# Kernel optimization log

Measured on AMD Instinct MI355X. Metric: run time of the kernel, lower is better.

Reference implementation:

```python
import jax, jax.numpy as jnp
import numpy as np

BS, D, NC, N, C, K = 8192, 1024, 64, 100000, 1000, 50


def setup_inputs() -> dict:
    key = jax.random.key(0)
    k1, k2, k3, k4, k5 = jax.random.split(key, 5)
    return {
        "train_embedding": jax.random.normal(k1, (BS, D), dtype=jnp.float32),
        # concept initialized uniform in [-0.5, 0.5] as in init_concept
        "concept": jax.random.uniform(k2, (D, NC), dtype=jnp.float32, minval=-0.5, maxval=0.5),
        "bank": jax.random.normal(k3, (N, D), dtype=jnp.float32),
        "W_h": jax.random.normal(k4, (D, C), dtype=jnp.float32) * 0.02,
        "b_h": jax.random.normal(k5, (C,), dtype=jnp.float32) * 0.02,
        "topk": K,
    }


def reference(train_embedding, concept, bank, W_h, b_h, topk):
    # h_x: linear classifier head
    def h_x(z):
        return z @ W_h + b_h

    # projection onto concept subspace: C (C^T C)^{-1} C^T
    G = concept.T @ concept                      # [nc, nc]
    proj_matrix = concept @ jnp.linalg.inv(G) @ concept.T  # [D, D]
    proj = train_embedding @ proj_matrix.T       # (proj_matrix @ X^T)^T -> [bs, D]
    y_pred = h_x(proj)                           # [bs, C]
    orig_pred = h_x(train_embedding)             # [bs, C]

    # batched per-concept Euclidean distance to the whole bank: [nc, N]
    bank_sq = jnp.sum(bank * bank, axis=1)       # [N]
    con_sq = jnp.sum(concept * concept, axis=0)  # [nc]
    d2 = con_sq[:, None] - 2.0 * (concept.T @ bank.T) + bank_sq[None, :]
    dist = jnp.sqrt(jnp.maximum(d2, 0.0))
    # topk SMALLEST distances per concept
    _, idx = jax.lax.top_k(-dist, topk)          # idx: [nc, k]
    knn = bank[idx]                              # [nc, k, D] gather

    # L_sparse_1: mean over concepts of (c . mean_k knn)
    dots = jnp.einsum('dn,nkd->n', concept, knn) / topk  # [nc]
    L_sparse_1 = jnp.mean(dots)

    nc = concept.shape[1]
    eye = jnp.eye(nc, dtype=concept.dtype)
    L_sparse_2 = jnp.mean(G * (1.0 - eye))       # off-diagonal mean
    norm_metrics = jnp.mean(G * eye)             # diagonal mean

    return (orig_pred, y_pred, L_sparse_1, L_sparse_2, norm_metrics)
```

## Files before the change

### kernel.cpp

```cpp
#include <hip/hip_runtime.h>
#include <cstddef>

#define BSZ   8192
#define DIM   1024
#define NCON  64
#define NBANK 100000
#define NCLS  1000
#define TOPK  50
#define NCHUNK 32
#define CHUNK  3125
#define CHUNKP 3328

#define Y_OFF 8192000
#define S_OFF 16384000

typedef __attribute__((ext_vector_type(8))) short bf16x8;
typedef __attribute__((ext_vector_type(4))) float f32x4;

__device__ __forceinline__ short f2bf(float x) {
    unsigned u = __builtin_bit_cast(unsigned, x);
    unsigned r = (u + 0x7fffu + ((u >> 16) & 1u)) >> 16;
    return (short)r;
}

__device__ __forceinline__ bf16x8 pack8(f32x4 a, f32x4 b) {
    bf16x8 p;
    p[0] = f2bf(a[0]); p[1] = f2bf(a[1]); p[2] = f2bf(a[2]); p[3] = f2bf(a[3]);
    p[4] = f2bf(b[0]); p[5] = f2bf(b[1]); p[6] = f2bf(b[2]); p[7] = f2bf(b[3]);
    return p;
}

__device__ __forceinline__ void gload16(const short* g, short* l) {
    __builtin_amdgcn_global_load_lds(
        (__attribute__((address_space(1))) void*)g,
        (__attribute__((address_space(3))) void*)l,
        16, 0, 0);
}

__global__ void __launch_bounds__(256) prep_kernel(const float* __restrict__ cpt,
                                                   const float* __restrict__ Wh,
                                                   short* __restrict__ WcatT,
                                                   short* __restrict__ cptT,
                                                   short* __restrict__ cptR) {
    __shared__ short Ts[64][65];
    int b = blockIdx.x;
    int t = threadIdx.x;
    if (b < 256) {
        int k0 = (b & 15) * 64, n0 = (b >> 4) * 64;
        #pragma unroll
        for (int i = 0; i < 16; ++i) {
            int u = i * 256 + t;
            int kL = u >> 6, nL = u & 63;
            int n = n0 + nL;
            Ts[kL][nL] = (n < NCLS) ? f2bf(Wh[(size_t)(k0 + kL) * NCLS + n]) : (short)0;
        }
        __syncthreads();
        #pragma unroll
        for (int i = 0; i < 16; ++i) {
            int u = i * 256 + t;
            int nL = u >> 6, kL = u & 63;
            WcatT[(size_t)(n0 + nL) * DIM + k0 + kL] = Ts[kL][nL];
        }
    } else {
        int q = b - 256;
        #pragma unroll
        for (int i = 0; i < 16; ++i) {
            int u = q * 4096 + i * 256 + t;
            int d = u >> 6, n = u & 63;
            short v = f2bf(cpt[u]);
            cptR[u] = v;
            cptT[n * DIM + d] = v;
        }
    }
}

__global__ void __launch_bounds__(256) mid_kernel(const float* __restrict__ bank,
                                                  const float* __restrict__ X,
                                                  const short* __restrict__ cptT,
                                                  const short* __restrict__ WcatT,
                                                  short* __restrict__ Xbf,
                                                  float* __restrict__ key,
                                                  float* __restrict__ bank_sq,
                                                  float* __restrict__ M,
                                                  float* __restrict__ G,
                                                  float* __restrict__ invG) {
    __shared__ float rowk[64];
    __shared__ float fk[64];
    int b = blockIdx.x;
    int t = threadIdx.x;
    int wid = t >> 6, l = t & 63, lr = l & 15, lg = l >> 4;
    if (b < 782) {
        int j0 = b * 128;
        int j_[2]; bool v_[2];
        const float* brow[2];
        #pragma unroll
        for (int ni = 0; ni < 2; ++ni) {
            j_[ni] = j0 + wid * 32 + ni * 16 + lr;
            v_[ni] = j_[ni] < NBANK;
            brow[ni] = bank + (size_t)j_[ni] * DIM + lg * 8;
        }
        f32x4 acc[4][2] = {};
        float sq[2] = {0.f, 0.f};
        for (int kk = 0; kk < DIM; kk += 32) {
            bf16x8 af[4];
            #pragma unroll
            for (int mi = 0; mi < 4; ++mi)
                af[mi] = *(const bf16x8*)(cptT + (mi * 16 + lr) * DIM + kk + lg * 8);
            #pragma unroll
            for (int ni = 0; ni < 2; ++ni) {
                f32x4 a = v_[ni] ? *(const f32x4*)(brow[ni] + kk)     : f32x4{0.f, 0.f, 0.f, 0.f};
                f32x4 c = v_[ni] ? *(const f32x4*)(brow[ni] + kk + 4) : f32x4{0.f, 0.f, 0.f, 0.f};
                sq[ni] += a[0]*a[0] + a[1]*a[1] + a[2]*a[2] + a[3]*a[3]
                        + c[0]*c[0] + c[1]*c[1] + c[2]*c[2] + c[3]*c[3];
                bf16x8 bfr = pack8(a, c);
                #pragma unroll
                for (int mi = 0; mi < 4; ++mi)
                    acc[mi][ni] = __builtin_amdgcn_mfma_f32_16x16x32_bf16(af[mi], bfr, acc[mi][ni], 0, 0, 0);
            }
        }
        #pragma unroll
        for (int ni = 0; ni < 2; ++ni) {
            float s = sq[ni];
            s += __shfl_xor(s, 16);
            s += __shfl_xor(s, 32);
            sq[ni] = s;
            if (v_[ni] && lg == 0) bank_sq[j_[ni]] = s;
        }
        #pragma unroll
        for (int mi = 0; mi < 4; ++mi)
            #pragma unroll
            for (int ni = 0; ni < 2; ++ni)
                if (v_[ni]) {
                    #pragma unroll
                    for (int r = 0; r < 4; ++r) {
                        int m = mi * 16 + lg * 4 + r;
                        key[(size_t)m * NBANK + j_[ni]] = sq[ni] - 2.f * acc[mi][ni][r];
                    }
                }
    } else if (b < 790) {
        int c0 = (b - 782) * 128;
        f32x4 acc[4][2] = {};
        for (int kk = 0; kk < DIM; kk += 32) {
            bf16x8 af[4], bfr[2];
            #pragma unroll
            for (int mi = 0; mi < 4; ++mi)
                af[mi] = *(const bf16x8*)(cptT + (mi * 16 + lr) * DIM + kk + lg * 8);
            #pragma unroll
            for (int ni = 0; ni < 2; ++ni)
                bfr[ni] = *(const bf16x8*)(WcatT + (size_t)(c0 + wid * 32 + ni * 16 + lr) * DIM + kk + lg * 8);
            #pragma unroll
            for (int mi = 0; mi < 4; ++mi)
                #pragma unroll
                for (int ni = 0; ni < 2; ++ni)
                    acc[mi][ni] = __builtin_amdgcn_mfma_f32_16x16x32_bf16(af[mi], bfr[ni], acc[mi][ni], 0, 0, 0);
        }
        #pragma unroll
        for (int mi = 0; mi < 4; ++mi)
            #pragma unroll
            for (int ni = 0; ni < 2; ++ni)
                #pragma unroll
                for (int r = 0; r < 4; ++r)
                    M[(mi * 16 + lg * 4 + r) * 1024 + c0 + wid * 32 + ni * 16 + lr] = acc[mi][ni][r];
    } else if (b == 790) {
        f32x4 acc[4] = {};
        for (int kk = 0; kk < DIM; kk += 32) {
            bf16x8 af[4], bfr;
            #pragma unroll
            for (int mi = 0; mi < 4; ++mi)
                af[mi] = *(const bf16x8*)(cptT + (mi * 16 + lr) * DIM + kk + lg * 8);
            bfr = *(const bf16x8*)(cptT + (wid * 16 + lr) * DIM + kk + lg * 8);
            #pragma unroll
            for (int mi = 0; mi < 4; ++mi)
                acc[mi] = __builtin_amdgcn_mfma_f32_16x16x32_bf16(af[mi], bfr, acc[mi], 0, 0, 0);
        }
        #pragma unroll
        for (int mi = 0; mi < 4; ++mi)
            #pragma unroll
            for (int r = 0; r < 4; ++r)
                G[(mi * 16 + lg * 4 + r) * 64 + wid * 16 + lr] = acc[mi][r];
        __syncthreads();
        float myA[16];
        #pragma unroll
        for (int s = 0; s < 16; ++s) myA[s] = G[(4 * s + wid) * 64 + l];
        #pragma unroll
        for (int k = 0; k < 64; ++k) {
            if (wid == (k & 3)) rowk[l] = myA[k >> 2];
            if (l == k) {
                #pragma unroll
                for (int s = 0; s < 16; ++s) fk[4 * s + wid] = myA[s];
            }
            __syncthreads();
            float ip = 1.f / rowk[k];
            float rv = rowk[l];
            #pragma unroll
            for (int s = 0; s < 16; ++s) {
                int i = 4 * s + wid;
                float fv = fk[i];
                float nv;
                if (i == k && l == k)      nv = ip;
                else if (i == k)           nv = rv * ip;
                else if (l == k)           nv = -fv * ip;
                else                       nv = myA[s] - fv * (rv * ip);
                myA[s] = nv;
            }
            __syncthreads();
        }
        #pragma unroll
        for (int s = 0; s < 16; ++s) invG[(4 * s + wid) * 64 + l] = myA[s];
    } else {
        size_t u = ((size_t)(b - 791) * 256 + t) * 8;
        f32x4 a = *(const f32x4*)(X + u);
        f32x4 c = *(const f32x4*)(X + u + 4);
        *(bf16x8*)(Xbf + u) = pack8(a, c);
    }
}

__global__ void __launch_bounds__(256) topA_kernel(const float* __restrict__ key,
                                                   float* __restrict__ cand_v,
                                                   int* __restrict__ cand_j) {
    int n = blockIdx.x >> 5;
    int c = blockIdx.x & 31;
    int base = c * CHUNK;
    const float* row = key + (size_t)n * NBANK + base;
    __shared__ float vals[CHUNKP];
    __shared__ float wv[4];
    __shared__ int wj[4];
    int t = threadIdx.x;
    float lv = __builtin_inff();
    int lj = 0x7fffffff;
    #pragma unroll 13
    for (int i = 0; i < 13; ++i) {
        int j = t + i * 256;
        float v = (j < CHUNK) ? row[j] : __builtin_inff();
        vals[j] = v;
        if (v < lv) { lv = v; lj = j; }
    }
    __syncthreads();
    float* cv = cand_v + (size_t)blockIdx.x * TOPK;
    int* cj = cand_j + (size_t)blockIdx.x * TOPK;
    for (int it = 0; it < TOPK; ++it) {
        float bv = lv; int bj = lj;
        #pragma unroll
        for (int o = 32; o > 0; o >>= 1) {
            float ov = __shfl_down(bv, o);
            int oj = __shfl_down(bj, o);
            if (ov < bv || (ov == bv && oj < bj)) { bv = ov; bj = oj; }
        }
        if ((t & 63) == 0) { wv[t >> 6] = bv; wj[t >> 6] = bj; }
        __syncthreads();
        float gv = wv[0]; int gj = wj[0];
        #pragma unroll
        for (int w = 1; w < 4; ++w)
            if (wv[w] < gv || (wv[w] == gv && wj[w] < gj)) { gv = wv[w]; gj = wj[w]; }
        if (t == 0) { cv[it] = gv; cj[it] = base + gj; }
        if (t == (gj & 255)) {
            vals[gj] = __builtin_inff();
            lv = __builtin_inff(); lj = 0x7fffffff;
            #pragma unroll 13
            for (int i = 0; i < 13; ++i) {
                int j = t + i * 256;
                float v = vals[j];
                if (v < lv) { lv = v; lj = j; }
            }
        }
        __syncthreads();
    }
}

__global__ void __launch_bounds__(256) m2w2_topB_kernel(const float* __restrict__ invG,
                                                        const float* __restrict__ M,
                                                        const short* __restrict__ cptR,
                                                        short* __restrict__ WcatT,
                                                        const float* __restrict__ cand_v,
                                                        const int* __restrict__ cand_j,
                                                        const float* __restrict__ bank_sq,
                                                        float* __restrict__ dots) {
    __shared__ __align__(16) char smem[49408];
    int b = blockIdx.x;
    int t = threadIdx.x;
    if (b < 8) {
        float* Mt = (float*)smem;
        short* M2s = (short*)(smem + 33024);
        int c0 = b * 128;
        for (int u = t; u < 8192; u += 256) {
            int j = u >> 7, cc = u & 127;
            Mt[j * 129 + cc] = M[j * 1024 + c0 + cc];
        }
        __syncthreads();
        int cl = t & 127, half = t >> 7;
        for (int nn = 0; nn < 32; ++nn) {
            int n = half * 32 + nn;
            float a = 0.f;
            #pragma unroll 16
            for (int j = 0; j < 64; ++j) a += invG[n * 64 + j] * Mt[j * 129 + cl];
            int s = n >> 3;
            M2s[cl * 64 + (((s ^ (cl & 7)) << 3) | (n & 7))] = f2bf(a);
        }
        __syncthreads();
        int wid = t >> 6, l = t & 63, lr = l & 15, lg = l >> 4;
        int wr = wid >> 1, wc = wid & 1;
        for (int d0 = 0; d0 < DIM; d0 += 128) {
            f32x4 acc[4][4] = {};
            #pragma unroll
            for (int ks = 0; ks < 2; ++ks) {
                bf16x8 af[4], bfr[4];
                #pragma unroll
                for (int mi = 0; mi < 4; ++mi) {
                    int rr = wr * 64 + mi * 16 + lr;
                    int slot = (ks * 4 + lg) ^ (rr & 7);
                    af[mi] = *(const bf16x8*)(M2s + rr * 64 + slot * 8);
                }
                #pragma unroll
                for (int ni = 0; ni < 4; ++ni)
                    bfr[ni] = *(const bf16x8*)(cptR + (size_t)(d0 + wc * 64 + ni * 16 + lr) * 64 + ks * 32 + lg * 8);
                #pragma unroll
                for (int mi = 0; mi < 4; ++mi)
                    #pragma unroll
                    for (int ni = 0; ni < 4; ++ni)
                        acc[mi][ni] = __builtin_amdgcn_mfma_f32_16x16x32_bf16(af[mi], bfr[ni], acc[mi][ni], 0, 0, 0);
            }
            #pragma unroll
            for (int mi = 0; mi < 4; ++mi)
                #pragma unroll
                for (int ni = 0; ni < 4; ++ni)
                    #pragma unroll
                    for (int r = 0; r < 4; ++r) {
                        int cc = c0 + wr * 64 + mi * 16 + lg * 4 + r;
                        int d = d0 + wc * 64 + ni * 16 + lr;
                        WcatT[(size_t)(1024 + cc) * DIM + d] = f2bf(acc[mi][ni][r]);
                    }
        }
    } else {
        int n = b - 8;
        const int NC2 = NCHUNK * TOPK;
        float* vals = (float*)smem;
        int* gidx = (int*)(smem + 6400);
        float* wv = (float*)(smem + 12800);
        int* wj = (int*)(smem + 12816);
        int* wl = (int*)(smem + 12832);
        for (int j = t; j < NC2; j += 256) {
            vals[j] = cand_v[(size_t)n * NC2 + j];
            gidx[j] = cand_j[(size_t)n * NC2 + j];
        }
        __syncthreads();
        float sum = 0.f;
        for (int it = 0; it < TOPK; ++it) {
            float bv = __builtin_inff();
            int bj = 0x7fffffff;
            int bl = -1;
            #pragma unroll 7
            for (int j = t; j < NC2; j += 256) {
                float v = vals[j];
                int gj = gidx[j];
                if (v < bv || (v == bv && gj < bj)) { bv = v; bj = gj; bl = j; }
            }
            #pragma unroll
            for (int o = 32; o > 0; o >>= 1) {
                float ov = __shfl_down(bv, o);
                int oj = __shfl_down(bj, o);
                int ol = __shfl_down(bl, o);
                if (ov < bv || (ov == bv && oj < bj)) { bv = ov; bj = oj; bl = ol; }
            }
            if ((t & 63) == 0) { wv[t >> 6] = bv; wj[t >> 6] = bj; wl[t >> 6] = bl; }
            __syncthreads();
            if (t == 0) {
                #pragma unroll
                for (int w = 1; w < 4; ++w)
                    if (wv[w] < bv || (wv[w] == bv && wj[w] < bj)) { bv = wv[w]; bj = wj[w]; bl = wl[w]; }
                sum += 0.5f * (bank_sq[bj] - bv);
                vals[bl] = __builtin_inff();
            }
            __syncthreads();
        }
        if (t == 0) dots[n] = sum / (float)TOPK;
    }
}

__global__ void __launch_bounds__(256) pred_fin_kernel(const short* __restrict__ Xbf,
                                                       const short* __restrict__ WcatT,
                                                       const float* __restrict__ bh,
                                                       const float* __restrict__ G,
                                                       const float* __restrict__ dots,
                                                       float* __restrict__ orig,
                                                       float* __restrict__ ypred,
                                                       float* __restrict__ out3) {
    __shared__ __align__(16) char smem[32768];
    int b = blockIdx.x;
    int t = threadIdx.x;
    if (b < 1024) {
        short* As = (short*)smem;
        short* Bs = (short*)(smem + 16384);
        int c0 = (b & 15) * 128;
        int r0 = (b >> 4) * 128;
        int wid = t >> 6, l = t & 63, lr = l & 15, lg = l >> 4;
        int wr = wid >> 1, wc = wid & 1;
        int srow_off = l >> 3;
        int scol = ((l & 7) ^ (l >> 3)) * 8;
        f32x4 acc[4][4] = {};
        for (int kk = 0; kk < DIM; kk += 64) {
            if (kk) __syncthreads();
            #pragma unroll
            for (int i = 0; i < 4; ++i) {
                int si = wid * 4 + i;
                int row = si * 8 + srow_off;
                gload16(Xbf + (size_t)(r0 + row) * DIM + kk + scol, As + si * 512);
                gload16(WcatT + (size_t)(c0 + row) * DIM + kk + scol, Bs + si * 512);
            }
            __syncthreads();
            #pragma unroll
            for (int ks = 0; ks < 2; ++ks) {
                bf16x8 af[4], bfr[4];
                #pragma unroll
                for (int mi = 0; mi < 4; ++mi) {
                    int rr = wr * 64 + mi * 16 + lr;
                    int slot = (ks * 4 + lg) ^ (rr & 7);
                    af[mi] = *(const bf16x8*)(As + rr * 64 + slot * 8);
                }
                #pragma unroll
                for (int ni = 0; ni < 4; ++ni) {
                    int cc = wc * 64 + ni * 16 + lr;
                    int slot = (ks * 4 + lg) ^ (cc & 7);
                    bfr[ni] = *(const bf16x8*)(Bs + cc * 64 + slot * 8);
                }
                #pragma unroll
                for (int mi = 0; mi < 4; ++mi)
                    #pragma unroll
                    for (int ni = 0; ni < 4; ++ni)
                        acc[mi][ni] = __builtin_amdgcn_mfma_f32_16x16x32_bf16(af[mi], bfr[ni], acc[mi][ni], 0, 0, 0);
            }
        }
        #pragma unroll
        for (int mi = 0; mi < 4; ++mi)
            #pragma unroll
            for (int ni = 0; ni < 4; ++ni) {
                int cg = c0 + wc * 64 + ni * 16 + lr;
                bool isorig = cg < NCLS;
                bool isy = (cg >= 1024) && (cg < 1024 + NCLS);
                if (isorig || isy) {
                    int cl = isorig ? cg : cg - 1024;
                    float bias = bh[cl];
                    float* dst = isorig ? orig : ypred;
                    #pragma unroll
                    for (int r = 0; r < 4; ++r) {
                        int row = r0 + wr * 64 + mi * 16 + lg * 4 + r;
                        dst[(size_t)row * NCLS + cl] = acc[mi][ni][r] + bias;
                    }
                }
            }
    } else {
        float* r1 = (float*)smem;
        float* r2 = (float*)(smem + 1024);
        float* r3 = (float*)(smem + 2048);
        float sd = 0.f, so = 0.f;
        for (int u = t; u < 4096; u += 256) {
            float g = G[u];
            if ((u >> 6) == (u & 63)) sd += g; else so += g;
        }
        float s1 = (t < NCON) ? dots[t] : 0.f;
        r1[t] = sd; r2[t] = so; r3[t] = s1;
        __syncthreads();
        for (int o = 128; o > 0; o >>= 1) {
            if (t < o) { r1[t] += r1[t + o]; r2[t] += r2[t + o]; r3[t] += r3[t + o]; }
            __syncthreads();
        }
        if (t == 0) {
            out3[0] = r3[0] / 64.f;
            out3[1] = r2[0] / 4096.f;
            out3[2] = r1[0] / 4096.f;
        }
    }
}

extern "C" void kernel_launch(void* const* d_in, const int* in_sizes, int n_in,
                              void* d_out, int out_size, void* d_ws, size_t ws_size,
                              hipStream_t stream) {
    const float* X    = (const float*)d_in[0];
    const float* cpt  = (const float*)d_in[1];
    const float* bank = (const float*)d_in[2];
    const float* Wh   = (const float*)d_in[3];
    const float* bh   = (const float*)d_in[4];
    float* out = (float*)d_out;

    float* orig  = out;
    float* ypred = out + Y_OFF;
    float* out3  = out + S_OFF;

    char* w = (char*)d_ws;
    short* Xbf    = (short*)(w);
    short* WcatT  = (short*)(w + 16777216);
    short* cptT   = (short*)(w + 20971520);
    short* cptR   = (short*)(w + 21102592);
    float* key    = (float*)(w + 21233664);
    float* bank_sq= (float*)(w + 46833664);
    float* G      = (float*)(w + 47234048);
    float* invG   = (float*)(w + 47250432);
    float* M      = (float*)(w + 47266816);
    float* cand_v = (float*)(w + 47528960);
    int*   cand_j = (int*)  (w + 47938560);
    float* dots   = (float*)(w + 48348160);

    prep_kernel<<<272, 256, 0, stream>>>(cpt, Wh, WcatT, cptT, cptR);
    mid_kernel<<<4887, 256, 0, stream>>>(bank, X, cptT, WcatT, Xbf, key, bank_sq, M, G, invG);
    topA_kernel<<<NCON * NCHUNK, 256, 0, stream>>>(key, cand_v, cand_j);
    m2w2_topB_kernel<<<72, 256, 0, stream>>>(invG, M, cptR, WcatT, cand_v, cand_j, bank_sq, dots);
    pred_fin_kernel<<<1025, 256, 0, stream>>>(Xbf, WcatT, bh, G, dots, orig, ypred, out3);
}
```

Baseline: 424.8 us.

## Compute y_pred via low-rank X·C then (invG·M) instead of a full D-wide projected GEMM

Instead of building a 1024-wide projected weight block (C·invG·C^T·W_h) and running the prediction GEMM over 2048 output columns, the code now computes X·C (rank 64) inside the X-to-bf16 conversion blocks. y_pred then comes from a small K=64 GEMM against invG·M. This roughly halves the big GEMM work, and the M2 computation is folded into the topA launch. It adds another bf16 rounding of the intermediate X·C and one extra small kernel launch for the final reductions.

```diff
diff --git a/kernel.cpp b/kernel.cpp
--- a/kernel.cpp
+++ b/kernel.cpp
@@ -39,9 +39,8 @@
 
 __global__ void __launch_bounds__(256) prep_kernel(const float* __restrict__ cpt,
                                                    const float* __restrict__ Wh,
-                                                   short* __restrict__ WcatT,
-                                                   short* __restrict__ cptT,
-                                                   short* __restrict__ cptR) {
+                                                   short* __restrict__ WhT,
+                                                   short* __restrict__ cptT) {
     __shared__ short Ts[64][65];
     int b = blockIdx.x;
     int t = threadIdx.x;
@@ -59,7 +58,7 @@
         for (int i = 0; i < 16; ++i) {
             int u = i * 256 + t;
             int nL = u >> 6, kL = u & 63;
-            WcatT[(size_t)(n0 + nL) * DIM + k0 + kL] = Ts[kL][nL];
+            WhT[(size_t)(n0 + nL) * DIM + k0 + kL] = Ts[kL][nL];
         }
     } else {
         int q = b - 256;
@@ -67,9 +66,7 @@
         for (int i = 0; i < 16; ++i) {
             int u = q * 4096 + i * 256 + t;
             int d = u >> 6, n = u & 63;
-            short v = f2bf(cpt[u]);
-            cptR[u] = v;
-            cptT[n * DIM + d] = v;
+            cptT[n * DIM + d] = f2bf(cpt[u]);
         }
     }
 }
@@ -77,8 +74,9 @@
 __global__ void __launch_bounds__(256) mid_kernel(const float* __restrict__ bank,
                                                   const float* __restrict__ X,
                                                   const short* __restrict__ cptT,
-                                                  const short* __restrict__ WcatT,
+                                                  const short* __restrict__ WhT,
                                                   short* __restrict__ Xbf,
+                                                  short* __restrict__ XCbf,
                                                   float* __restrict__ key,
                                                   float* __restrict__ bank_sq,
                                                   float* __restrict__ M,
@@ -147,7 +145,7 @@
                 af[mi] = *(const bf16x8*)(cptT + (mi * 16 + lr) * DIM + kk + lg * 8);
             #pragma unroll
             for (int ni = 0; ni < 2; ++ni)
-                bfr[ni] = *(const bf16x8*)(WcatT + (size_t)(c0 + wid * 32 + ni * 16 + lr) * DIM + kk + lg * 8);
+                bfr[ni] = *(const bf16x8*)(WhT + (size_t)(c0 + wid * 32 + ni * 16 + lr) * DIM + kk + lg * 8);
             #pragma unroll
             for (int mi = 0; mi < 4; ++mi)
                 #pragma unroll
@@ -208,80 +206,102 @@
         #pragma unroll
         for (int s = 0; s < 16; ++s) invG[(4 * s + wid) * 64 + l] = myA[s];
     } else {
-        size_t u = ((size_t)(b - 791) * 256 + t) * 8;
-        f32x4 a = *(const f32x4*)(X + u);
-        f32x4 c = *(const f32x4*)(X + u + 4);
-        *(bf16x8*)(Xbf + u) = pack8(a, c);
+        int r0 = (b - 791) * 128;
+        int r_[2];
+        const float* xrow[2];
+        #pragma unroll
+        for (int ni = 0; ni < 2; ++ni) {
+            r_[ni] = r0 + wid * 32 + ni * 16 + lr;
+            xrow[ni] = X + (size_t)r_[ni] * DIM + lg * 8;
+        }
+        f32x4 acc[4][2] = {};
+        for (int kk = 0; kk < DIM; kk += 32) {
+            bf16x8 af[4];
+            #pragma unroll
+            for (int mi = 0; mi < 4; ++mi)
+                af[mi] = *(const bf16x8*)(cptT + (mi * 16 + lr) * DIM + kk + lg * 8);
+            #pragma unroll
+            for (int ni = 0; ni < 2; ++ni) {
+                f32x4 a = *(const f32x4*)(xrow[ni] + kk);
+                f32x4 c = *(const f32x4*)(xrow[ni] + kk + 4);
+                bf16x8 pk = pack8(a, c);
+                *(bf16x8*)(Xbf + (size_t)r_[ni] * DIM + kk + lg * 8) = pk;
+                #pragma unroll
+                for (int mi = 0; mi < 4; ++mi)
+                    acc[mi][ni] = __builtin_amdgcn_mfma_f32_16x16x32_bf16(af[mi], pk, acc[mi][ni], 0, 0, 0);
+            }
+        }
+        #pragma unroll
+        for (int mi = 0; mi < 4; ++mi)
+            #pragma unroll
+            for (int ni = 0; ni < 2; ++ni)
+                #pragma unroll
+                for (int r = 0; r < 4; ++r) {
+                    int m = mi * 16 + lg * 4 + r;
+                    XCbf[(size_t)r_[ni] * NCON + m] = f2bf(acc[mi][ni][r]);
+                }
     }
 }
 
 __global__ void __launch_bounds__(256) topA_kernel(const float* __restrict__ key,
                                                    float* __restrict__ cand_v,
-                                                   int* __restrict__ cand_j) {
-    int n = blockIdx.x >> 5;
-    int c = blockIdx.x & 31;
-    int base = c * CHUNK;
-    const float* row = key + (size_t)n * NBANK + base;
-    __shared__ float vals[CHUNKP];
-    __shared__ float wv[4];
-    __shared__ int wj[4];
-    int t = threadIdx.x;
-    float lv = __builtin_inff();
-    int lj = 0x7fffffff;
-    #pragma unroll 13
-    for (int i = 0; i < 13; ++i) {
-        int j = t + i * 256;
-        float v = (j < CHUNK) ? row[j] : __builtin_inff();
-        vals[j] = v;
-        if (v < lv) { lv = v; lj = j; }
-    }
-    __syncthreads();
-    float* cv = cand_v + (size_t)blockIdx.x * TOPK;
-    int* cj = cand_j + (size_t)blockIdx.x * TOPK;
-    for (int it = 0; it < TOPK; ++it) {
-        float bv = lv; int bj = lj;
-        #pragma unroll
-        for (int o = 32; o > 0; o >>= 1) {
-            float ov = __shfl_down(bv, o);
-            int oj = __shfl_down(bj, o);
-            if (ov < bv || (ov == bv && oj < bj)) { bv = ov; bj = oj; }
-        }
-        if ((t & 63) == 0) { wv[t >> 6] = bv; wj[t >> 6] = bj; }
-        __syncthreads();
-        float gv = wv[0]; int gj = wj[0];
-        #pragma unroll
-        for (int w = 1; w < 4; ++w)
-            if (wv[w] < gv || (wv[w] == gv && wj[w] < gj)) { gv = wv[w]; gj = wj[w]; }
-        if (t == 0) { cv[it] = gv; cj[it] = base + gj; }
-        if (t == (gj & 255)) {
-            vals[gj] = __builtin_inff();
-            lv = __builtin_inff(); lj = 0x7fffffff;
-            #pragma unroll 13
-            for (int i = 0; i < 13; ++i) {
-                int j = t + i * 256;
-                float v = vals[j];
-                if (v < lv) { lv = v; lj = j; }
-            }
-        }
-        __syncthreads();
-    }
-}
-
-__global__ void __launch_bounds__(256) m2w2_topB_kernel(const float* __restrict__ invG,
-                                                        const float* __restrict__ M,
-                                                        const short* __restrict__ cptR,
-                                                        short* __restrict__ WcatT,
-                                                        const float* __restrict__ cand_v,
-                                                        const int* __restrict__ cand_j,
-                                                        const float* __restrict__ bank_sq,
-                                                        float* __restrict__ dots) {
-    __shared__ __align__(16) char smem[49408];
+                                                   int* __restrict__ cand_j,
+                                                   const float* __restrict__ invG,
+                                                   const float* __restrict__ M,
+                                                   short* __restrict__ M2T) {
+    __shared__ __align__(16) char smem[33280];
     int b = blockIdx.x;
     int t = threadIdx.x;
-    if (b < 8) {
+    if (b < 2048) {
+        float* vals = (float*)smem;
+        float* wv = (float*)(smem + 13312);
+        int* wj = (int*)(smem + 13328);
+        int n = b >> 5;
+        int c = b & 31;
+        int base = c * CHUNK;
+        const float* row = key + (size_t)n * NBANK + base;
+        float lv = __builtin_inff();
+        int lj = 0x7fffffff;
+        #pragma unroll 13
+        for (int i = 0; i < 13; ++i) {
+            int j = t + i * 256;
+            float v = (j < CHUNK) ? row[j] : __builtin_inff();
+            vals[j] = v;
+            if (v < lv) { lv = v; lj = j; }
+        }
+        __syncthreads();
+        float* cv = cand_v + (size_t)b * TOPK;
+        int* cj = cand_j + (size_t)b * TOPK;
+        for (int it = 0; it < TOPK; ++it) {
+            float bv = lv; int bj = lj;
+            #pragma unroll
+            for (int o = 32; o > 0; o >>= 1) {
+                float ov = __shfl_down(bv, o);
+                int oj = __shfl_down(bj, o);
+                if (ov < bv || (ov == bv && oj < bj)) { bv = ov; bj = oj; }
+            }
+            if ((t & 63) == 0) { wv[t >> 6] = bv; wj[t >> 6] = bj; }
+            __syncthreads();
+            float gv = wv[0]; int gj = wj[0];
+            #pragma unroll
+            for (int w2 = 1; w2 < 4; ++w2)
+                if (wv[w2] < gv || (wv[w2] == gv && wj[w2] < gj)) { gv = wv[w2]; gj = wj[w2]; }
+            if (t == 0) { cv[it] = gv; cj[it] = base + gj; }
+            if (t == (gj & 255)) {
+                vals[gj] = __builtin_inff();
+                lv = __builtin_inff(); lj = 0x7fffffff;
+                #pragma unroll 13
+                for (int i = 0; i < 13; ++i) {
+                    int j = t + i * 256;
+                    float v = vals[j];
+                    if (v < lv) { lv = v; lj = j; }
+                }
+            }
+            __syncthreads();
+        }
+    } else {
         float* Mt = (float*)smem;
-        short* M2s = (short*)(smem + 33024);
-        int c0 = b * 128;
+        int c0 = (b - 2048) * 128;
         for (int u = t; u < 8192; u += 256) {
             int j = u >> 7, cc = u & 127;
             Mt[j * 129 + cc] = M[j * 1024 + c0 + cc];
@@ -293,14 +313,45 @@
             float a = 0.f;
             #pragma unroll 16
             for (int j = 0; j < 64; ++j) a += invG[n * 64 + j] * Mt[j * 129 + cl];
-            int s = n >> 3;
-            M2s[cl * 64 + (((s ^ (cl & 7)) << 3) | (n & 7))] = f2bf(a);
-        }
-        __syncthreads();
-        int wid = t >> 6, l = t & 63, lr = l & 15, lg = l >> 4;
+            M2T[(size_t)(c0 + cl) * NCON + n] = f2bf(a);
+        }
+    }
+}
+
+__global__ void __launch_bounds__(256) pred_kernel(const short* __restrict__ Xbf,
+                                                   const short* __restrict__ WhT,
+                                                   const short* __restrict__ XCbf,
+                                                   const short* __restrict__ M2T,
+                                                   const float* __restrict__ bh,
+                                                   const float* __restrict__ cand_v,
+                                                   const int* __restrict__ cand_j,
+                                                   const float* __restrict__ bank_sq,
+                                                   float* __restrict__ orig,
+                                                   float* __restrict__ ypred,
+                                                   float* __restrict__ dots) {
+    __shared__ __align__(16) char smem[32768];
+    int b = blockIdx.x;
+    int t = threadIdx.x;
+    int wid = t >> 6, l = t & 63, lr = l & 15, lg = l >> 4;
+    if (b < 512) {
+        short* As = (short*)smem;
+        short* Bs = (short*)(smem + 16384);
+        int c0 = (b & 7) * 128;
+        int r0 = (b >> 3) * 128;
         int wr = wid >> 1, wc = wid & 1;
-        for (int d0 = 0; d0 < DIM; d0 += 128) {
-            f32x4 acc[4][4] = {};
+        int srow_off = l >> 3;
+        int scol = ((l & 7) ^ (l >> 3)) * 8;
+        f32x4 acc[4][4] = {};
+        for (int kk = 0; kk < DIM; kk += 64) {
+            if (kk) __syncthreads();
+            #pragma unroll
+            for (int i = 0; i < 4; ++i) {
+                int si = wid * 4 + i;
+                int row = si * 8 + srow_off;
+                gload16(Xbf + (size_t)(r0 + row) * DIM + kk + scol, As + si * 512);
+                gload16(WhT + (size_t)(c0 + row) * DIM + kk + scol, Bs + si * 512);
+            }
+            __syncthreads();
             #pragma unroll
             for (int ks = 0; ks < 2; ++ks) {
                 bf16x8 af[4], bfr[4];
@@ -308,30 +359,72 @@
                 for (int mi = 0; mi < 4; ++mi) {
                     int rr = wr * 64 + mi * 16 + lr;
                     int slot = (ks * 4 + lg) ^ (rr & 7);
-                    af[mi] = *(const bf16x8*)(M2s + rr * 64 + slot * 8);
-                }
-                #pragma unroll
-                for (int ni = 0; ni < 4; ++ni)
-                    bfr[ni] = *(const bf16x8*)(cptR + (size_t)(d0 + wc * 64 + ni * 16 + lr) * 64 + ks * 32 + lg * 8);
+                    af[mi] = *(const bf16x8*)(As + rr * 64 + slot * 8);
+                }
+                #pragma unroll
+                for (int ni = 0; ni < 4; ++ni) {
+                    int cc = wc * 64 + ni * 16 + lr;
+                    int slot = (ks * 4 + lg) ^ (cc & 7);
+                    bfr[ni] = *(const bf16x8*)(Bs + cc * 64 + slot * 8);
+                }
                 #pragma unroll
                 for (int mi = 0; mi < 4; ++mi)
                     #pragma unroll
                     for (int ni = 0; ni < 4; ++ni)
                         acc[mi][ni] = __builtin_amdgcn_mfma_f32_16x16x32_bf16(af[mi], bfr[ni], acc[mi][ni], 0, 0, 0);
             }
-            #pragma unroll
-            for (int mi = 0; mi < 4; ++mi)
-                #pragma unroll
-                for (int ni = 0; ni < 4; ++ni)
+        }
+        #pragma unroll
+        for (int mi = 0; mi < 4; ++mi)
+            #pragma unroll
+            for (int ni = 0; ni < 4; ++ni) {
+                int col = c0 + wc * 64 + ni * 16 + lr;
+                if (col < NCLS) {
+                    float bias = bh[col];
                     #pragma unroll
                     for (int r = 0; r < 4; ++r) {
-                        int cc = c0 + wr * 64 + mi * 16 + lg * 4 + r;
-                        int d = d0 + wc * 64 + ni * 16 + lr;
-                        WcatT[(size_t)(1024 + cc) * DIM + d] = f2bf(acc[mi][ni][r]);
+                        int row = r0 + wr * 64 + mi * 16 + lg * 4 + r;
+                        orig[(size_t)row * NCLS + col] = acc[mi][ni][r] + bias;
                     }
-        }
+                }
+            }
+    } else if (b < 1024) {
+        int q = b - 512;
+        int c0 = (q & 7) * 128;
+        int r0 = (q >> 3) * 128;
+        int wr = wid >> 1, wc = wid & 1;
+        f32x4 acc[4][4] = {};
+        #pragma unroll
+        for (int ks = 0; ks < 2; ++ks) {
+            bf16x8 af[4], bfr[4];
+            #pragma unroll
+            for (int mi = 0; mi < 4; ++mi)
+                af[mi] = *(const bf16x8*)(XCbf + (size_t)(r0 + wr * 64 + mi * 16 + lr) * NCON + ks * 32 + lg * 8);
+            #pragma unroll
+            for (int ni = 0; ni < 4; ++ni)
+                bfr[ni] = *(const bf16x8*)(M2T + (size_t)(c0 + wc * 64 + ni * 16 + lr) * NCON + ks * 32 + lg * 8);
+            #pragma unroll
+            for (int mi = 0; mi < 4; ++mi)
+                #pragma unroll
+                for (int ni = 0; ni < 4; ++ni)
+                    acc[mi][ni] = __builtin_amdgcn_mfma_f32_16x16x32_bf16(af[mi], bfr[ni], acc[mi][ni], 0, 0, 0);
+        }
+        #pragma unroll
+        for (int mi = 0; mi < 4; ++mi)
+            #pragma unroll
+            for (int ni = 0; ni < 4; ++ni) {
+                int col = c0 + wc * 64 + ni * 16 + lr;
+                if (col < NCLS) {
+                    float bias = bh[col];
+                    #pragma unroll
+                    for (int r = 0; r < 4; ++r) {
+                        int row = r0 + wr * 64 + mi * 16 + lg * 4 + r;
+                        ypred[(size_t)row * NCLS + col] = acc[mi][ni][r] + bias;
+                    }
+                }
+            }
     } else {
-        int n = b - 8;
+        int n = b - 1024;
         const int NC2 = NCHUNK * TOPK;
         float* vals = (float*)smem;
         int* gidx = (int*)(smem + 6400);
@@ -365,8 +458,8 @@
             __syncthreads();
             if (t == 0) {
                 #pragma unroll
-                for (int w = 1; w < 4; ++w)
-                    if (wv[w] < bv || (wv[w] == bv && wj[w] < bj)) { bv = wv[w]; bj = wj[w]; bl = wl[w]; }
+                for (int w2 = 1; w2 < 4; ++w2)
+                    if (wv[w2] < bv || (wv[w2] == bv && wj[w2] < bj)) { bv = wv[w2]; bj = wj[w2]; bl = wl[w2]; }
                 sum += 0.5f * (bank_sq[bj] - bv);
                 vals[bl] = __builtin_inff();
             }
@@ -376,98 +469,27 @@
     }
 }
 
-__global__ void __launch_bounds__(256) pred_fin_kernel(const short* __restrict__ Xbf,
-                                                       const short* __restrict__ WcatT,
-                                                       const float* __restrict__ bh,
-                                                       const float* __restrict__ G,
-                                                       const float* __restrict__ dots,
-                                                       float* __restrict__ orig,
-                                                       float* __restrict__ ypred,
-                                                       float* __restrict__ out3) {
-    __shared__ __align__(16) char smem[32768];
-    int b = blockIdx.x;
+__global__ void __launch_bounds__(256) fin_kernel(const float* __restrict__ G,
+                                                  const float* __restrict__ dots,
+                                                  float* __restrict__ out3) {
+    __shared__ float r1[256], r2[256], r3[256];
     int t = threadIdx.x;
-    if (b < 1024) {
-        short* As = (short*)smem;
-        short* Bs = (short*)(smem + 16384);
-        int c0 = (b & 15) * 128;
-        int r0 = (b >> 4) * 128;
-        int wid = t >> 6, l = t & 63, lr = l & 15, lg = l >> 4;
-        int wr = wid >> 1, wc = wid & 1;
-        int srow_off = l >> 3;
-        int scol = ((l & 7) ^ (l >> 3)) * 8;
-        f32x4 acc[4][4] = {};
-        for (int kk = 0; kk < DIM; kk += 64) {
-            if (kk) __syncthreads();
-            #pragma unroll
-            for (int i = 0; i < 4; ++i) {
-                int si = wid * 4 + i;
-                int row = si * 8 + srow_off;
-                gload16(Xbf + (size_t)(r0 + row) * DIM + kk + scol, As + si * 512);
-                gload16(WcatT + (size_t)(c0 + row) * DIM + kk + scol, Bs + si * 512);
-            }
-            __syncthreads();
-            #pragma unroll
-            for (int ks = 0; ks < 2; ++ks) {
-                bf16x8 af[4], bfr[4];
-                #pragma unroll
-                for (int mi = 0; mi < 4; ++mi) {
-                    int rr = wr * 64 + mi * 16 + lr;
-                    int slot = (ks * 4 + lg) ^ (rr & 7);
-                    af[mi] = *(const bf16x8*)(As + rr * 64 + slot * 8);
-                }
-                #pragma unroll
-                for (int ni = 0; ni < 4; ++ni) {
-                    int cc = wc * 64 + ni * 16 + lr;
-                    int slot = (ks * 4 + lg) ^ (cc & 7);
-                    bfr[ni] = *(const bf16x8*)(Bs + cc * 64 + slot * 8);
-                }
-                #pragma unroll
-                for (int mi = 0; mi < 4; ++mi)
-                    #pragma unroll
-                    for (int ni = 0; ni < 4; ++ni)
-                        acc[mi][ni] = __builtin_amdgcn_mfma_f32_16x16x32_bf16(af[mi], bfr[ni], acc[mi][ni], 0, 0, 0);
-            }
-        }
-        #pragma unroll
-        for (int mi = 0; mi < 4; ++mi)
-            #pragma unroll
-            for (int ni = 0; ni < 4; ++ni) {
-                int cg = c0 + wc * 64 + ni * 16 + lr;
-                bool isorig = cg < NCLS;
-                bool isy = (cg >= 1024) && (cg < 1024 + NCLS);
-                if (isorig || isy) {
-                    int cl = isorig ? cg : cg - 1024;
-                    float bias = bh[cl];
-                    float* dst = isorig ? orig : ypred;
-                    #pragma unroll
-                    for (int r = 0; r < 4; ++r) {
-                        int row = r0 + wr * 64 + mi * 16 + lg * 4 + r;
-                        dst[(size_t)row * NCLS + cl] = acc[mi][ni][r] + bias;
-                    }
-                }
-            }
-    } else {
-        float* r1 = (float*)smem;
-        float* r2 = (float*)(smem + 1024);
-        float* r3 = (float*)(smem + 2048);
-        float sd = 0.f, so = 0.f;
-        for (int u = t; u < 4096; u += 256) {
-            float g = G[u];
-            if ((u >> 6) == (u & 63)) sd += g; else so += g;
-        }
-        float s1 = (t < NCON) ? dots[t] : 0.f;
-        r1[t] = sd; r2[t] = so; r3[t] = s1;
+    float sd = 0.f, so = 0.f;
+    for (int u = t; u < 4096; u += 256) {
+        float g = G[u];
+        if ((u >> 6) == (u & 63)) sd += g; else so += g;
+    }
+    float s1 = (t < NCON) ? dots[t] : 0.f;
+    r1[t] = sd; r2[t] = so; r3[t] = s1;
+    __syncthreads();
+    for (int o = 128; o > 0; o >>= 1) {
+        if (t < o) { r1[t] += r1[t + o]; r2[t] += r2[t + o]; r3[t] += r3[t + o]; }
         __syncthreads();
-        for (int o = 128; o > 0; o >>= 1) {
-            if (t < o) { r1[t] += r1[t + o]; r2[t] += r2[t + o]; r3[t] += r3[t + o]; }
-            __syncthreads();
-        }
-        if (t == 0) {
-            out3[0] = r3[0] / 64.f;
-            out3[1] = r2[0] / 4096.f;
-            out3[2] = r1[0] / 4096.f;
-        }
+    }
+    if (t == 0) {
+        out3[0] = r3[0] / 64.f;
+        out3[1] = r2[0] / 4096.f;
+        out3[2] = r1[0] / 4096.f;
     }
 }
 
@@ -487,21 +509,22 @@
 
     char* w = (char*)d_ws;
     short* Xbf    = (short*)(w);
-    short* WcatT  = (short*)(w + 16777216);
-    short* cptT   = (short*)(w + 20971520);
-    short* cptR   = (short*)(w + 21102592);
-    float* key    = (float*)(w + 21233664);
-    float* bank_sq= (float*)(w + 46833664);
-    float* G      = (float*)(w + 47234048);
-    float* invG   = (float*)(w + 47250432);
-    float* M      = (float*)(w + 47266816);
-    float* cand_v = (float*)(w + 47528960);
-    int*   cand_j = (int*)  (w + 47938560);
-    float* dots   = (float*)(w + 48348160);
-
-    prep_kernel<<<272, 256, 0, stream>>>(cpt, Wh, WcatT, cptT, cptR);
-    mid_kernel<<<4887, 256, 0, stream>>>(bank, X, cptT, WcatT, Xbf, key, bank_sq, M, G, invG);
-    topA_kernel<<<NCON * NCHUNK, 256, 0, stream>>>(key, cand_v, cand_j);
-    m2w2_topB_kernel<<<72, 256, 0, stream>>>(invG, M, cptR, WcatT, cand_v, cand_j, bank_sq, dots);
-    pred_fin_kernel<<<1025, 256, 0, stream>>>(Xbf, WcatT, bh, G, dots, orig, ypred, out3);
-}
+    short* WhT    = (short*)(w + 16777216);
+    short* cptT   = (short*)(w + 18874368);
+    short* XCbf   = (short*)(w + 19005440);
+    short* M2T    = (short*)(w + 20054016);
+    float* key    = (float*)(w + 20185088);
+    float* bank_sq= (float*)(w + 45785088);
+    float* G      = (float*)(w + 46185472);
+    float* invG   = (float*)(w + 46201856);
+    float* M      = (float*)(w + 46218240);
+    float* cand_v = (float*)(w + 46480384);
+    int*   cand_j = (int*)  (w + 46889984);
+    float* dots   = (float*)(w + 47299584);
+
+    prep_kernel<<<272, 256, 0, stream>>>(cpt, Wh, WhT, cptT);
+    mid_kernel<<<855, 256, 0, stream>>>(bank, X, cptT, WhT, Xbf, XCbf, key, bank_sq, M, G, invG);
+    topA_kernel<<<2056, 256, 0, stream>>>(key, cand_v, cand_j, invG, M, M2T);
+    pred_kernel<<<1088, 256, 0, stream>>>(Xbf, WhT, XCbf, M2T, bh, cand_v, cand_j, bank_sq, orig, ypred, dots);
+    fin_kernel<<<1, 256, 0, stream>>>(G, dots, out3);
+}
```

Measured after the change: 451.4 us. 6.2% more time.
